# Kernel tuning notes

Measured on AMD Instinct MI355X. Metric: run time of the kernel, lower is better.

## Reference

```python
import math
import jax, jax.numpy as jnp
import numpy as np

N = 50000          # nodes
E = 800000         # edges
IN_DIM = 128
HID = 128
OUT_DIM = 64
LAYER_NUM = 8      # -> LAYER_NUM - 2 = 6 GCN2Conv layers
NUM_CONVS = LAYER_NUM - 2
ALPHA = 0.1
THETA = 0.5
# PyG GCN2Conv: beta = log(theta / layer + 1); here every conv was built with layer = layer_num + 1
BETA = math.log(THETA / (LAYER_NUM + 1) + 1.0)


def setup_inputs() -> dict:
    key = jax.random.key(0)
    ks = jax.random.split(key, 10)
    x = jax.random.normal(ks[0], (N, IN_DIM), dtype=jnp.float32)
    edge_src = jax.random.randint(ks[1], (E,), 0, N, dtype=jnp.int32)
    edge_dst = jax.random.randint(ks[2], (E,), 0, N, dtype=jnp.int32)
    edge_weight = jax.random.uniform(ks[3], (E,), dtype=jnp.float32)
    s0 = 1.0 / math.sqrt(IN_DIM)
    s1 = 1.0 / math.sqrt(HID)
    W0 = jax.random.uniform(ks[4], (IN_DIM, HID), dtype=jnp.float32, minval=-s0, maxval=s0)
    b0 = jnp.zeros((HID,), dtype=jnp.float32)
    W1 = jax.random.uniform(ks[5], (HID, OUT_DIM), dtype=jnp.float32, minval=-s1, maxval=s1)
    b1 = jnp.zeros((OUT_DIM,), dtype=jnp.float32)
    conv_ws = jax.random.uniform(ks[6], (NUM_CONVS, HID, HID), dtype=jnp.float32, minval=-s1, maxval=s1)
    return {"x": x, "edge_src": edge_src, "edge_dst": edge_dst, "edge_weight": edge_weight,
            "W0": W0, "b0": b0, "W1": W1, "b1": b1, "conv_ws": conv_ws}


def reference(x, edge_src, edge_dst, edge_weight, W0, b0, W1, b1, conv_ws):
    # linear[0] + relu (dropout=0.0 -> identity)
    h = jnp.maximum(x @ W0 + b0, 0.0)          # [N, HID]
    x0 = h
    for i in range(NUM_CONVS):
        # weighted neighbor sum: out[i] = sum_{(j->i)} w_ji * h[j]
        msgs = h[edge_src] * edge_weight[:, None]               # [E, HID]
        agg = jax.ops.segment_sum(msgs, edge_dst, num_segments=N)
        # GCN2Conv (shared_weights=True): z = (1-alpha)*Ah + alpha*x0; out = (1-beta)*z + beta*(z W)
        z = agg * (1.0 - ALPHA) + ALPHA * x0
        h = z * (1.0 - BETA) + BETA * (z @ conv_ws[i])
        h = jnp.maximum(h, 0.0)
    return h @ W1 + b1                          # [N, OUT_DIM]
```

## Files before the change

kernel.cpp:

```cpp
#include <hip/hip_runtime.h>
#include <cstdint>
#include <cstddef>


#define NN 50000
#define EE 800000

constexpr float ALPHA   = 0.1f;
constexpr float BETA_C  = 0.05406722127027574f;

constexpr int NB = (NN + 255) / 256;
constexpr int HB = (EE + 255) / 256;
constexpr int PREP_TOT = 128 * 128 + 6 * 128 * 128 + 64 * 128;
constexpr int PB = (PREP_TOT + 255) / 256;
constexpr int SLICE = NN / 8;
constexpr int GA = (NN + 63) / 64;
constexpr int AGGB = 8 * ((GA + 1) / 2);

typedef unsigned short u16;
typedef unsigned int   u32;
typedef __attribute__((ext_vector_type(8))) short short8;
typedef __attribute__((ext_vector_type(4))) float f32x4;

__device__ __forceinline__ float bf2f(u16 u) {
    union { float f; u32 i; } c; c.i = ((u32)u) << 16; return c.f;
}
__device__ __forceinline__ u16 f2bf(float f) {
    union { float f; u32 i; } c; c.f = f;
    u32 r = c.i + 0x7fffu + ((c.i >> 16) & 1u);
    return (u16)(r >> 16);
}

__global__ void k_hist_prep(const int* __restrict__ edst, int* __restrict__ deg,
                            const float* __restrict__ W0, const float* __restrict__ cw,
                            const float* __restrict__ W1, u16* __restrict__ w0t,
                            u16* __restrict__ wft, u16* __restrict__ w1t, int E) {
    int b = blockIdx.x;
    if (b < HB) {
        int i = b * 256 + threadIdx.x;
        if (i < E) atomicAdd(&deg[edst[i]], 1);
    } else {
        int i = (b - HB) * 256 + threadIdx.x;
        if (i < 16384) {
            int n = i >> 7, k = i & 127;
            w0t[i] = f2bf(W0[k * 128 + n]);
        } else if (i < 16384 + 6 * 16384) {
            int r = i - 16384;
            int l = r >> 14; int t = r & 16383;
            int n = t >> 7, k = t & 127;
            float v = BETA_C * cw[l * 16384 + k * 128 + n]
                      + ((k == n) ? (1.f - BETA_C) : 0.f);
            wft[r] = f2bf(v);
        } else if (i < PREP_TOT) {
            int r = i - (16384 + 6 * 16384);
            int n = r >> 7, k = r & 127;
            w1t[r] = f2bf(W1[k * 64 + n]);
        }
    }
}

__global__ __launch_bounds__(256) void k_scan_lb(const int* __restrict__ deg,
                                                 int* __restrict__ bsum,
                                                 int* __restrict__ offs,
                                                 int* __restrict__ cur) {
    __shared__ int sh[256];
    __shared__ int sw[4];
    const int c = blockIdx.x, tid = threadIdx.x;
    const int i = c * 256 + tid;
    int v = (i < NN) ? deg[i] : 0;
    sh[tid] = v;
    __syncthreads();
#pragma unroll
    for (int o = 1; o < 256; o <<= 1) {
        int u = (tid >= o) ? sh[tid - o] : 0;
        __syncthreads();
        sh[tid] += u;
        __syncthreads();
    }
    if (tid == 255) atomicExch(&bsum[c], sh[255] + 1);
    int part = 0;
    for (int t = tid; t < c; t += 256) {
        int b;
        do { b = atomicAdd(&bsum[t], 0); } while (b == 0);
        part += b - 1;
    }
#pragma unroll
    for (int o = 32; o > 0; o >>= 1) part += __shfl_down(part, o);
    if ((tid & 63) == 0) sw[tid >> 6] = part;
    __syncthreads();
    const int base = sw[0] + sw[1] + sw[2] + sw[3];
    const int ex = base + sh[tid] - v;
    if (i < NN) {
        offs[i] = ex;
        cur[i]  = ex;
        if (i == NN - 1) offs[NN] = ex + v;
    }
}

__device__ __forceinline__ void gemm0_tile(int t, const float* __restrict__ x,
                                           const u16* __restrict__ w0t,
                                           const float* __restrict__ b0,
                                           u16* __restrict__ x0s) {
    const int lane = threadIdx.x & 63;
    const int wave = threadIdx.x >> 6;
    const int q = lane >> 4;
    const int m16 = lane & 15;
    const int node = t * 64 + wave * 16 + m16;
    const int nload = node < NN ? node : NN - 1;

    short8 zf[4];
    const float* xp = x + (size_t)nload * 128 + q * 8;
#pragma unroll
    for (int s = 0; s < 4; ++s) {
        float4 u0 = *(const float4*)(xp + s * 32);
        float4 u1 = *(const float4*)(xp + s * 32 + 4);
        short8 z;
        z[0] = (short)f2bf(u0.x); z[1] = (short)f2bf(u0.y);
        z[2] = (short)f2bf(u0.z); z[3] = (short)f2bf(u0.w);
        z[4] = (short)f2bf(u1.x); z[5] = (short)f2bf(u1.y);
        z[6] = (short)f2bf(u1.z); z[7] = (short)f2bf(u1.w);
        zf[s] = z;
    }

    f32x4 acc[8];
#pragma unroll
    for (int c = 0; c < 8; ++c) {
        f32x4 a = {0.f, 0.f, 0.f, 0.f};
        const u16* wp = w0t + (size_t)(c * 16 + m16) * 128 + q * 8;
#pragma unroll
        for (int s = 0; s < 4; ++s) {
            short8 wf = *(const short8*)(wp + s * 32);
            a = __builtin_amdgcn_mfma_f32_16x16x32_bf16(wf, zf[s], a, 0, 0, 0);
        }
        acc[c] = a;
    }

    if (node < NN) {
#pragma unroll
        for (int c = 0; c < 8; ++c) {
            const int f0 = c * 16 + q * 4;
            float4 bv = *(const float4*)(b0 + f0);
            float v0 = acc[c][0] + bv.x; v0 = v0 > 0.f ? v0 : 0.f;
            float v1 = acc[c][1] + bv.y; v1 = v1 > 0.f ? v1 : 0.f;
            float v2 = acc[c][2] + bv.z; v2 = v2 > 0.f ? v2 : 0.f;
            float v3 = acc[c][3] + bv.w; v3 = v3 > 0.f ? v3 : 0.f;
            ushort4 o;
            o.x = f2bf(v0); o.y = f2bf(v1); o.z = f2bf(v2); o.w = f2bf(v3);
            *(ushort4*)(x0s + (size_t)(f0 >> 5) * NN * 32
                        + (size_t)node * 32 + (f0 & 31)) = o;
        }
    }
}

__global__ __launch_bounds__(256) void k_bucket_g0(const int* __restrict__ src,
                                                   const int* __restrict__ dst,
                                                   const float* __restrict__ w,
                                                   int* __restrict__ cur,
                                                   u32* __restrict__ ep,
                                                   const float* __restrict__ x,
                                                   const u16* __restrict__ w0t,
                                                   const float* __restrict__ b0,
                                                   u16* __restrict__ x0s, int E) {
    const int b = blockIdx.x;
    if (b < HB * 8) {
        const int slice = b & 7;
        const int i = (b >> 3) * 256 + threadIdx.x;
        if (i >= E) return;
        const int d = dst[i];
        const int lo = slice * SLICE;
        if (d >= lo && d < lo + SLICE) {
            int pos = atomicAdd(&cur[d], 1);
            ep[pos] = ((u32)f2bf(w[i]) << 16) | (u32)src[i];
        }
    } else {
        gemm0_tile(b - HB * 8, x, w0t, b0, x0s);
    }
}

__global__ __launch_bounds__(256) void k_agg_z(const int* __restrict__ offs,
                                               const u32* __restrict__ ep,
                                               const u16* __restrict__ hs,
                                               const u16* __restrict__ x0s,
                                               u16* __restrict__ zs) {
    const int bid = blockIdx.x;
    const int s     = (bid & 7) >> 1;
    const int chunk = ((bid >> 3) << 1) | (bid & 1);
    const int lane = threadIdx.x & 63;
    const int wave = threadIdx.x >> 6;
    const int g  = lane >> 2;
    const int f4 = lane & 3;
    const int n  = chunk * 64 + wave * 16 + g;
    const int nc = n < NN ? n : NN - 1;
    const uint4* table = (const uint4*)(hs + (size_t)s * NN * 32);

    const int beg = offs[nc], end = offs[nc + 1];
    float a0 = 0.f, a1 = 0.f, a2 = 0.f, a3 = 0.f;
    float a4 = 0.f, a5 = 0.f, a6 = 0.f, a7 = 0.f;
    int e = beg;
    for (; e + 7 < end; e += 8) {
        u32 r[8]; uint4 v[8];
#pragma unroll
        for (int j = 0; j < 8; ++j) r[j] = ep[e + j];
#pragma unroll
        for (int j = 0; j < 8; ++j)
            v[j] = table[(size_t)(r[j] & 0xffffu) * 4 + f4];
#pragma unroll
        for (int j = 0; j < 8; ++j) {
            float w = bf2f((u16)(r[j] >> 16));
            a0 += w * bf2f((u16)v[j].x);  a1 += w * bf2f((u16)(v[j].x >> 16));
            a2 += w * bf2f((u16)v[j].y);  a3 += w * bf2f((u16)(v[j].y >> 16));
            a4 += w * bf2f((u16)v[j].z);  a5 += w * bf2f((u16)(v[j].z >> 16));
            a6 += w * bf2f((u16)v[j].w);  a7 += w * bf2f((u16)(v[j].w >> 16));
        }
    }
    for (; e < end; ++e) {
        u32 r = ep[e];
        uint4 v = table[(size_t)(r & 0xffffu) * 4 + f4];
        float w = bf2f((u16)(r >> 16));
        a0 += w * bf2f((u16)v.x);  a1 += w * bf2f((u16)(v.x >> 16));
        a2 += w * bf2f((u16)v.y);  a3 += w * bf2f((u16)(v.y >> 16));
        a4 += w * bf2f((u16)v.z);  a5 += w * bf2f((u16)(v.z >> 16));
        a6 += w * bf2f((u16)v.w);  a7 += w * bf2f((u16)(v.w >> 16));
    }
    if (n < NN) {
        const size_t idx = (size_t)s * NN * 4 + (size_t)n * 4 + f4;
        uint4 xv = ((const uint4*)x0s)[idx];
        float z0 = (1.f - ALPHA) * a0 + ALPHA * bf2f((u16)xv.x);
        float z1 = (1.f - ALPHA) * a1 + ALPHA * bf2f((u16)(xv.x >> 16));
        float z2 = (1.f - ALPHA) * a2 + ALPHA * bf2f((u16)xv.y);
        float z3 = (1.f - ALPHA) * a3 + ALPHA * bf2f((u16)(xv.y >> 16));
        float z4 = (1.f - ALPHA) * a4 + ALPHA * bf2f((u16)xv.z);
        float z5 = (1.f - ALPHA) * a5 + ALPHA * bf2f((u16)(xv.z >> 16));
        float z6 = (1.f - ALPHA) * a6 + ALPHA * bf2f((u16)xv.w);
        float z7 = (1.f - ALPHA) * a7 + ALPHA * bf2f((u16)(xv.w >> 16));
        uint4 o;
        o.x = (u32)f2bf(z0) | ((u32)f2bf(z1) << 16);
        o.y = (u32)f2bf(z2) | ((u32)f2bf(z3) << 16);
        o.z = (u32)f2bf(z4) | ((u32)f2bf(z5) << 16);
        o.w = (u32)f2bf(z6) | ((u32)f2bf(z7) << 16);
        ((uint4*)zs)[idx] = o;
    }
}

__global__ __launch_bounds__(256) void k_gemm_conv(const u16* __restrict__ z,
                                                   const u16* __restrict__ Wt,
                                                   u16* __restrict__ hout) {
    const int lane = threadIdx.x & 63;
    const int wave = threadIdx.x >> 6;
    const int q = lane >> 4;
    const int m16 = lane & 15;
    const int node = blockIdx.x * 64 + wave * 16 + m16;
    const int nload = node < NN ? node : NN - 1;

    short8 zf[4];
#pragma unroll
    for (int s = 0; s < 4; ++s)
        zf[s] = *(const short8*)(z + (size_t)s * NN * 32 + (size_t)nload * 32 + q * 8);

    f32x4 acc[8];
#pragma unroll
    for (int c = 0; c < 8; ++c) {
        f32x4 a = {0.f, 0.f, 0.f, 0.f};
        const u16* wp = Wt + (size_t)(c * 16 + m16) * 128 + q * 8;
#pragma unroll
        for (int s = 0; s < 4; ++s) {
            short8 wf = *(const short8*)(wp + s * 32);
            a = __builtin_amdgcn_mfma_f32_16x16x32_bf16(wf, zf[s], a, 0, 0, 0);
        }
        acc[c] = a;
    }

    if (node < NN) {
#pragma unroll
        for (int c = 0; c < 8; ++c) {
            const int f0 = c * 16 + q * 4;
            float v0 = acc[c][0] > 0.f ? acc[c][0] : 0.f;
            float v1 = acc[c][1] > 0.f ? acc[c][1] : 0.f;
            float v2 = acc[c][2] > 0.f ? acc[c][2] : 0.f;
            float v3 = acc[c][3] > 0.f ? acc[c][3] : 0.f;
            ushort4 o;
            o.x = f2bf(v0); o.y = f2bf(v1); o.z = f2bf(v2); o.w = f2bf(v3);
            *(ushort4*)(hout + (size_t)(f0 >> 5) * NN * 32
                        + (size_t)node * 32 + (f0 & 31)) = o;
        }
    }
}

__global__ __launch_bounds__(256) void k_gemm_last(const u16* __restrict__ z,
                                                   const u16* __restrict__ wf5,
                                                   const u16* __restrict__ w1t,
                                                   const float* __restrict__ b1,
                                                   float* __restrict__ out) {
    __shared__ __align__(16) u16 hl[4][16][136];
    const int lane = threadIdx.x & 63;
    const int wave = threadIdx.x >> 6;
    const int q = lane >> 4;
    const int m16 = lane & 15;
    const int node = blockIdx.x * 64 + wave * 16 + m16;
    const int nload = node < NN ? node : NN - 1;

    short8 zf[4];
#pragma unroll
    for (int s = 0; s < 4; ++s)
        zf[s] = *(const short8*)(z + (size_t)s * NN * 32 + (size_t)nload * 32 + q * 8);

#pragma unroll
    for (int c = 0; c < 8; ++c) {
        f32x4 a = {0.f, 0.f, 0.f, 0.f};
        const u16* wp = wf5 + (size_t)(c * 16 + m16) * 128 + q * 8;
#pragma unroll
        for (int s = 0; s < 4; ++s) {
            short8 wf = *(const short8*)(wp + s * 32);
            a = __builtin_amdgcn_mfma_f32_16x16x32_bf16(wf, zf[s], a, 0, 0, 0);
        }
        float v0 = a[0] > 0.f ? a[0] : 0.f;
        float v1 = a[1] > 0.f ? a[1] : 0.f;
        float v2 = a[2] > 0.f ? a[2] : 0.f;
        float v3 = a[3] > 0.f ? a[3] : 0.f;
        ushort4 o;
        o.x = f2bf(v0); o.y = f2bf(v1); o.z = f2bf(v2); o.w = f2bf(v3);
        *(ushort4*)&hl[wave][m16][c * 16 + q * 4] = o;
    }
    __syncthreads();

    short8 hf[4];
#pragma unroll
    for (int s = 0; s < 4; ++s)
        hf[s] = *(const short8*)&hl[wave][m16][s * 32 + q * 8];

#pragma unroll
    for (int c = 0; c < 4; ++c) {
        f32x4 a = {0.f, 0.f, 0.f, 0.f};
        const u16* wp = w1t + (size_t)(c * 16 + m16) * 128 + q * 8;
#pragma unroll
        for (int s = 0; s < 4; ++s) {
            short8 wf = *(const short8*)(wp + s * 32);
            a = __builtin_amdgcn_mfma_f32_16x16x32_bf16(wf, hf[s], a, 0, 0, 0);
        }
        if (node < NN) {
            const int f0 = c * 16 + q * 4;
            float4 bv = *(const float4*)(b1 + f0);
            float4 o;
            o.x = a[0] + bv.x; o.y = a[1] + bv.y;
            o.z = a[2] + bv.z; o.w = a[3] + bv.w;
            *(float4*)(out + (size_t)node * 64 + f0) = o;
        }
    }
}


extern "C" void kernel_launch(void* const* d_in, const int* in_sizes, int n_in,
                              void* d_out, int out_size, void* d_ws, size_t ws_size,
                              hipStream_t stream) {
    const float* x    = (const float*)d_in[0];
    const int*   esrc = (const int*)d_in[1];
    const int*   edst = (const int*)d_in[2];
    const float* ew   = (const float*)d_in[3];
    const float* W0   = (const float*)d_in[4];
    const float* b0   = (const float*)d_in[5];
    const float* W1   = (const float*)d_in[6];
    const float* b1   = (const float*)d_in[7];
    const float* cw   = (const float*)d_in[8];
    float* out = (float*)d_out;

    u32* ep4 = (u32*)d_ws;
    u16* x0s = (u16*)(ep4 + EE);
    u16* hb1 = x0s + (size_t)4 * NN * 32;
    u16* hb2 = hb1 + (size_t)4 * NN * 32;
    u16* zsb = hb2 + (size_t)4 * NN * 32;
    u16* w0t = zsb + (size_t)4 * NN * 32;
    u16* wft = w0t + 128 * 128;
    u16* w1t = wft + 6 * 128 * 128;
    int* deg = (int*)(w1t + 64 * 128);
    int* bsum = deg + NN;
    int* offs = bsum + NB;
    int* cur = offs + NN + 1;

    (void)hipMemsetAsync(deg, 0, (size_t)(NN + NB) * sizeof(int), stream);
    k_hist_prep<<<HB + PB, 256, 0, stream>>>(edst, deg, W0, cw, W1, w0t, wft, w1t, EE);
    k_scan_lb<<<NB, 256, 0, stream>>>(deg, bsum, offs, cur);
    k_bucket_g0<<<HB * 8 + GA, 256, 0, stream>>>(esrc, edst, ew, cur, ep4,
                                                 x, w0t, b0, x0s, EE);

    const u16* hin = x0s;
    u16* houts[5] = {hb1, hb2, hb1, hb2, hb1};
    for (int i = 0; i < 5; ++i) {
        k_agg_z<<<AGGB, 256, 0, stream>>>(offs, ep4, hin, x0s, zsb);
        k_gemm_conv<<<GA, 256, 0, stream>>>(zsb, wft + (size_t)i * 16384, houts[i]);
        hin = houts[i];
    }

    k_agg_z<<<AGGB, 256, 0, stream>>>(offs, ep4, hin, x0s, zsb);
    k_gemm_last<<<GA, 256, 0, stream>>>(zsb, wft + (size_t)5 * 16384, w1t, b1, out);
}
```

Before: 501.5 us.

## Fuse neighbor aggregation into the conv GEMM kernel via register fragments

Merges the separate aggregation kernel and GEMM kernel into one. Each lane gathers its node's neighbor rows for its q-slice across all four feature slabs and builds the MFMA B-fragment directly in registers, so the z intermediate is never written to or reread from global memory and one launch per layer is removed. The trade-off is less parallelism in the gather phase: the old aggregation used 8x more blocks with 4 lanes per node per slab, while now 4 lanes cover a node across all slabs and the unroll drops from 8 to 2 edges. That may expose more gather latency and raise register pressure.

```diff
diff --git a/kernel.cpp b/kernel.cpp
--- a/kernel.cpp
+++ b/kernel.cpp
@@ -15,12 +15,12 @@
 constexpr int PB = (PREP_TOT + 255) / 256;
 constexpr int SLICE = NN / 8;
 constexpr int GA = (NN + 63) / 64;
-constexpr int AGGB = 8 * ((GA + 1) / 2);
 
 typedef unsigned short u16;
 typedef unsigned int   u32;
 typedef __attribute__((ext_vector_type(8))) short short8;
 typedef __attribute__((ext_vector_type(4))) float f32x4;
+typedef __attribute__((ext_vector_type(4))) u32   u32x4;
 
 __device__ __forceinline__ float bf2f(u16 u) {
     union { float f; u32 i; } c; c.i = ((u32)u) << 16; return c.f;
@@ -177,85 +177,88 @@
     }
 }
 
-__global__ __launch_bounds__(256) void k_agg_z(const int* __restrict__ offs,
-                                               const u32* __restrict__ ep,
-                                               const u16* __restrict__ hs,
-                                               const u16* __restrict__ x0s,
-                                               u16* __restrict__ zs) {
-    const int bid = blockIdx.x;
-    const int s     = (bid & 7) >> 1;
-    const int chunk = ((bid >> 3) << 1) | (bid & 1);
-    const int lane = threadIdx.x & 63;
-    const int wave = threadIdx.x >> 6;
-    const int g  = lane >> 2;
-    const int f4 = lane & 3;
-    const int n  = chunk * 64 + wave * 16 + g;
-    const int nc = n < NN ? n : NN - 1;
-    const uint4* table = (const uint4*)(hs + (size_t)s * NN * 32);
-
+__device__ __forceinline__ void agg_z_frag(const int* __restrict__ offs,
+                                           const u32* __restrict__ ep,
+                                           const u16* __restrict__ hs,
+                                           const u16* __restrict__ x0s,
+                                           int nc, int q, short8* zf) {
     const int beg = offs[nc], end = offs[nc + 1];
-    float a0 = 0.f, a1 = 0.f, a2 = 0.f, a3 = 0.f;
-    float a4 = 0.f, a5 = 0.f, a6 = 0.f, a7 = 0.f;
+    float acc[4][8];
+#pragma unroll
+    for (int s = 0; s < 4; ++s)
+#pragma unroll
+        for (int j = 0; j < 8; ++j) acc[s][j] = 0.f;
+
+    const u16* base = hs + q * 8;
     int e = beg;
-    for (; e + 7 < end; e += 8) {
-        u32 r[8]; uint4 v[8];
-#pragma unroll
-        for (int j = 0; j < 8; ++j) r[j] = ep[e + j];
-#pragma unroll
-        for (int j = 0; j < 8; ++j)
-            v[j] = table[(size_t)(r[j] & 0xffffu) * 4 + f4];
-#pragma unroll
-        for (int j = 0; j < 8; ++j) {
-            float w = bf2f((u16)(r[j] >> 16));
-            a0 += w * bf2f((u16)v[j].x);  a1 += w * bf2f((u16)(v[j].x >> 16));
-            a2 += w * bf2f((u16)v[j].y);  a3 += w * bf2f((u16)(v[j].y >> 16));
-            a4 += w * bf2f((u16)v[j].z);  a5 += w * bf2f((u16)(v[j].z >> 16));
-            a6 += w * bf2f((u16)v[j].w);  a7 += w * bf2f((u16)(v[j].w >> 16));
+    for (; e + 1 < end; e += 2) {
+        u32 r0 = ep[e], r1 = ep[e + 1];
+        const u16* p0 = base + (size_t)(r0 & 0xffffu) * 32;
+        const u16* p1 = base + (size_t)(r1 & 0xffffu) * 32;
+        u32x4 v0[4], v1[4];
+#pragma unroll
+        for (int s = 0; s < 4; ++s) {
+            v0[s] = *(const u32x4*)(p0 + (size_t)s * NN * 32);
+            v1[s] = *(const u32x4*)(p1 + (size_t)s * NN * 32);
+        }
+        float w0 = bf2f((u16)(r0 >> 16));
+        float w1 = bf2f((u16)(r1 >> 16));
+#pragma unroll
+        for (int s = 0; s < 4; ++s) {
+#pragma unroll
+            for (int u = 0; u < 4; ++u) {
+                acc[s][2 * u]     += w0 * bf2f((u16)v0[s][u]);
+                acc[s][2 * u + 1] += w0 * bf2f((u16)(v0[s][u] >> 16));
+                acc[s][2 * u]     += w1 * bf2f((u16)v1[s][u]);
+                acc[s][2 * u + 1] += w1 * bf2f((u16)(v1[s][u] >> 16));
+            }
         }
     }
     for (; e < end; ++e) {
         u32 r = ep[e];
-        uint4 v = table[(size_t)(r & 0xffffu) * 4 + f4];
+        const u16* p = base + (size_t)(r & 0xffffu) * 32;
         float w = bf2f((u16)(r >> 16));
-        a0 += w * bf2f((u16)v.x);  a1 += w * bf2f((u16)(v.x >> 16));
-        a2 += w * bf2f((u16)v.y);  a3 += w * bf2f((u16)(v.y >> 16));
-        a4 += w * bf2f((u16)v.z);  a5 += w * bf2f((u16)(v.z >> 16));
-        a6 += w * bf2f((u16)v.w);  a7 += w * bf2f((u16)(v.w >> 16));
-    }
-    if (n < NN) {
-        const size_t idx = (size_t)s * NN * 4 + (size_t)n * 4 + f4;
-        uint4 xv = ((const uint4*)x0s)[idx];
-        float z0 = (1.f - ALPHA) * a0 + ALPHA * bf2f((u16)xv.x);
-        float z1 = (1.f - ALPHA) * a1 + ALPHA * bf2f((u16)(xv.x >> 16));
-        float z2 = (1.f - ALPHA) * a2 + ALPHA * bf2f((u16)xv.y);
-        float z3 = (1.f - ALPHA) * a3 + ALPHA * bf2f((u16)(xv.y >> 16));
-        float z4 = (1.f - ALPHA) * a4 + ALPHA * bf2f((u16)xv.z);
-        float z5 = (1.f - ALPHA) * a5 + ALPHA * bf2f((u16)(xv.z >> 16));
-        float z6 = (1.f - ALPHA) * a6 + ALPHA * bf2f((u16)xv.w);
-        float z7 = (1.f - ALPHA) * a7 + ALPHA * bf2f((u16)(xv.w >> 16));
-        uint4 o;
-        o.x = (u32)f2bf(z0) | ((u32)f2bf(z1) << 16);
-        o.y = (u32)f2bf(z2) | ((u32)f2bf(z3) << 16);
-        o.z = (u32)f2bf(z4) | ((u32)f2bf(z5) << 16);
-        o.w = (u32)f2bf(z6) | ((u32)f2bf(z7) << 16);
-        ((uint4*)zs)[idx] = o;
-    }
-}
-
-__global__ __launch_bounds__(256) void k_gemm_conv(const u16* __restrict__ z,
-                                                   const u16* __restrict__ Wt,
-                                                   u16* __restrict__ hout) {
+#pragma unroll
+        for (int s = 0; s < 4; ++s) {
+            u32x4 v = *(const u32x4*)(p + (size_t)s * NN * 32);
+#pragma unroll
+            for (int u = 0; u < 4; ++u) {
+                acc[s][2 * u]     += w * bf2f((u16)v[u]);
+                acc[s][2 * u + 1] += w * bf2f((u16)(v[u] >> 16));
+            }
+        }
+    }
+
+#pragma unroll
+    for (int s = 0; s < 4; ++s) {
+        u32x4 xv = *(const u32x4*)(x0s + (size_t)s * NN * 32 + (size_t)nc * 32 + q * 8);
+        short8 z;
+#pragma unroll
+        for (int u = 0; u < 4; ++u) {
+            float zl = (1.f - ALPHA) * acc[s][2 * u]     + ALPHA * bf2f((u16)xv[u]);
+            float zh = (1.f - ALPHA) * acc[s][2 * u + 1] + ALPHA * bf2f((u16)(xv[u] >> 16));
+            z[2 * u]     = (short)f2bf(zl);
+            z[2 * u + 1] = (short)f2bf(zh);
+        }
+        zf[s] = z;
+    }
+}
+
+__global__ __launch_bounds__(256) void k_agg_gemm(const int* __restrict__ offs,
+                                                  const u32* __restrict__ ep,
+                                                  const u16* __restrict__ hs,
+                                                  const u16* __restrict__ x0s,
+                                                  const u16* __restrict__ Wt,
+                                                  u16* __restrict__ hout) {
     const int lane = threadIdx.x & 63;
     const int wave = threadIdx.x >> 6;
     const int q = lane >> 4;
     const int m16 = lane & 15;
     const int node = blockIdx.x * 64 + wave * 16 + m16;
-    const int nload = node < NN ? node : NN - 1;
+    const int nc = node < NN ? node : NN - 1;
 
     short8 zf[4];
-#pragma unroll
-    for (int s = 0; s < 4; ++s)
-        zf[s] = *(const short8*)(z + (size_t)s * NN * 32 + (size_t)nload * 32 + q * 8);
+    agg_z_frag(offs, ep, hs, x0s, nc, q, zf);
 
     f32x4 acc[8];
 #pragma unroll
@@ -286,23 +289,24 @@
     }
 }
 
-__global__ __launch_bounds__(256) void k_gemm_last(const u16* __restrict__ z,
-                                                   const u16* __restrict__ wf5,
-                                                   const u16* __restrict__ w1t,
-                                                   const float* __restrict__ b1,
-                                                   float* __restrict__ out) {
+__global__ __launch_bounds__(256) void k_agg_gemm_last(const int* __restrict__ offs,
+                                                       const u32* __restrict__ ep,
+                                                       const u16* __restrict__ hs,
+                                                       const u16* __restrict__ x0s,
+                                                       const u16* __restrict__ wf5,
+                                                       const u16* __restrict__ w1t,
+                                                       const float* __restrict__ b1,
+                                                       float* __restrict__ out) {
     __shared__ __align__(16) u16 hl[4][16][136];
     const int lane = threadIdx.x & 63;
     const int wave = threadIdx.x >> 6;
     const int q = lane >> 4;
     const int m16 = lane & 15;
     const int node = blockIdx.x * 64 + wave * 16 + m16;
-    const int nload = node < NN ? node : NN - 1;
+    const int nc = node < NN ? node : NN - 1;
 
     short8 zf[4];
-#pragma unroll
-    for (int s = 0; s < 4; ++s)
-        zf[s] = *(const short8*)(z + (size_t)s * NN * 32 + (size_t)nload * 32 + q * 8);
+    agg_z_frag(offs, ep, hs, x0s, nc, q, zf);
 
 #pragma unroll
     for (int c = 0; c < 8; ++c) {
@@ -385,11 +389,11 @@
     const u16* hin = x0s;
     u16* houts[5] = {hb1, hb2, hb1, hb2, hb1};
     for (int i = 0; i < 5; ++i) {
-        k_agg_z<<<AGGB, 256, 0, stream>>>(offs, ep4, hin, x0s, zsb);
-        k_gemm_conv<<<GA, 256, 0, stream>>>(zsb, wft + (size_t)i * 16384, houts[i]);
+        k_agg_gemm<<<GA, 256, 0, stream>>>(offs, ep4, hin, x0s,
+                                           wft + (size_t)i * 16384, houts[i]);
         hin = houts[i];
     }
 
-    k_agg_z<<<AGGB, 256, 0, stream>>>(offs, ep4, hin, x0s, zsb);
-    k_gemm_last<<<GA, 256, 0, stream>>>(zsb, wft + (size_t)5 * 16384, w1t, b1, out);
-}
+    k_agg_gemm_last<<<GA, 256, 0, stream>>>(offs, ep4, hin, x0s,
+                                            wft + (size_t)5 * 16384, w1t, b1, out);
+}
```

Measured after the change: 615.4 us. 1.23x slower.

## Sort nodes by in-degree to balance aggregation work across wavefront lanes

Applied to the files above, without the earlier changes.

Builds a degree histogram during the scan, then a new placement kernel counting-sorts node ids by in-degree into an order array. The aggregation kernel processes nodes in this order, so lanes of the same wave handle nodes with similar edge counts and diverge less in their loops. In exchange it adds an extra kernel launch and one indirection per node. The z writes and x0 reads become scattered rather than contiguous, which may hurt memory coalescing.

```diff
diff --git a/kernel.cpp b/kernel.cpp
--- a/kernel.cpp
+++ b/kernel.cpp
@@ -62,12 +62,14 @@
 __global__ __launch_bounds__(256) void k_scan_lb(const int* __restrict__ deg,
                                                  int* __restrict__ bsum,
                                                  int* __restrict__ offs,
-                                                 int* __restrict__ cur) {
+                                                 int* __restrict__ cur,
+                                                 int* __restrict__ binCnt) {
     __shared__ int sh[256];
     __shared__ int sw[4];
     const int c = blockIdx.x, tid = threadIdx.x;
     const int i = c * 256 + tid;
     int v = (i < NN) ? deg[i] : 0;
+    if (i < NN) atomicAdd(&binCnt[v > 255 ? 255 : v], 1);
     sh[tid] = v;
     __syncthreads();
 #pragma unroll
@@ -94,6 +96,34 @@
         offs[i] = ex;
         cur[i]  = ex;
         if (i == NN - 1) offs[NN] = ex + v;
+    }
+}
+
+__global__ __launch_bounds__(256) void k_place(const int* __restrict__ deg,
+                                               const int* __restrict__ binCnt,
+                                               int* __restrict__ binCur,
+                                               int* __restrict__ order) {
+    __shared__ int sh[256];
+    __shared__ int eb[256];
+    const int tid = threadIdx.x;
+    const int cnt = binCnt[tid];
+    sh[tid] = cnt;
+    __syncthreads();
+#pragma unroll
+    for (int o = 1; o < 256; o <<= 1) {
+        int u = (tid >= o) ? sh[tid - o] : 0;
+        __syncthreads();
+        sh[tid] += u;
+        __syncthreads();
+    }
+    eb[tid] = sh[tid] - cnt;
+    __syncthreads();
+    const int i = blockIdx.x * 256 + tid;
+    if (i < NN) {
+        int d = deg[i];
+        int bin = d > 255 ? 255 : d;
+        int pos = eb[bin] + atomicAdd(&binCur[bin], 1);
+        order[pos] = i;
     }
 }
 
@@ -181,7 +211,8 @@
                                                const u32* __restrict__ ep,
                                                const u16* __restrict__ hs,
                                                const u16* __restrict__ x0s,
-                                               u16* __restrict__ zs) {
+                                               u16* __restrict__ zs,
+                                               const int* __restrict__ order) {
     const int bid = blockIdx.x;
     const int s     = (bid & 7) >> 1;
     const int chunk = ((bid >> 3) << 1) | (bid & 1);
@@ -189,8 +220,9 @@
     const int wave = threadIdx.x >> 6;
     const int g  = lane >> 2;
     const int f4 = lane & 3;
-    const int n  = chunk * 64 + wave * 16 + g;
-    const int nc = n < NN ? n : NN - 1;
+    const int n0 = chunk * 64 + wave * 16 + g;
+    const int ni = n0 < NN ? n0 : NN - 1;
+    const int nc = order[ni];
     const uint4* table = (const uint4*)(hs + (size_t)s * NN * 32);
 
     const int beg = offs[nc], end = offs[nc + 1];
@@ -222,8 +254,8 @@
         a4 += w * bf2f((u16)v.z);  a5 += w * bf2f((u16)(v.z >> 16));
         a6 += w * bf2f((u16)v.w);  a7 += w * bf2f((u16)(v.w >> 16));
     }
-    if (n < NN) {
-        const size_t idx = (size_t)s * NN * 4 + (size_t)n * 4 + f4;
+    if (n0 < NN) {
+        const size_t idx = (size_t)s * NN * 4 + (size_t)nc * 4 + f4;
         uint4 xv = ((const uint4*)x0s)[idx];
         float z0 = (1.f - ALPHA) * a0 + ALPHA * bf2f((u16)xv.x);
         float z1 = (1.f - ALPHA) * a1 + ALPHA * bf2f((u16)(xv.x >> 16));
@@ -373,23 +405,27 @@
     u16* w1t = wft + 6 * 128 * 128;
     int* deg = (int*)(w1t + 64 * 128);
     int* bsum = deg + NN;
-    int* offs = bsum + NB;
-    int* cur = offs + NN + 1;
-
-    (void)hipMemsetAsync(deg, 0, (size_t)(NN + NB) * sizeof(int), stream);
+    int* binCnt = bsum + NB;
+    int* binCur = binCnt + 256;
+    int* offs = binCur + 256;
+    int* cur  = offs + NN + 1;
+    int* order = cur + NN;
+
+    (void)hipMemsetAsync(deg, 0, (size_t)(NN + NB + 512) * sizeof(int), stream);
     k_hist_prep<<<HB + PB, 256, 0, stream>>>(edst, deg, W0, cw, W1, w0t, wft, w1t, EE);
-    k_scan_lb<<<NB, 256, 0, stream>>>(deg, bsum, offs, cur);
+    k_scan_lb<<<NB, 256, 0, stream>>>(deg, bsum, offs, cur, binCnt);
+    k_place<<<NB, 256, 0, stream>>>(deg, binCnt, binCur, order);
     k_bucket_g0<<<HB * 8 + GA, 256, 0, stream>>>(esrc, edst, ew, cur, ep4,
                                                  x, w0t, b0, x0s, EE);
 
     const u16* hin = x0s;
     u16* houts[5] = {hb1, hb2, hb1, hb2, hb1};
     for (int i = 0; i < 5; ++i) {
-        k_agg_z<<<AGGB, 256, 0, stream>>>(offs, ep4, hin, x0s, zsb);
+        k_agg_z<<<AGGB, 256, 0, stream>>>(offs, ep4, hin, x0s, zsb, order);
         k_gemm_conv<<<GA, 256, 0, stream>>>(zsb, wft + (size_t)i * 16384, houts[i]);
         hin = houts[i];
     }
 
-    k_agg_z<<<AGGB, 256, 0, stream>>>(offs, ep4, hin, x0s, zsb);
+    k_agg_z<<<AGGB, 256, 0, stream>>>(offs, ep4, hin, x0s, zsb, order);
     k_gemm_last<<<GA, 256, 0, stream>>>(zsb, wft + (size_t)5 * 16384, w1t, b1, out);
 }
```

Measured after the change: 800.3 us. 1.6x slower.
